# Optimization experiments

Measured on AMD Instinct MI355X. Metric: run time of the kernel, lower is better.

## Reference

```python
import jax, jax.numpy as jnp
import numpy as np

NUM_EMBEDDINGS = 8192
EMBEDDING_DIM = 256
COMMITMENT_COST = 0.25


def setup_inputs() -> dict:
    key = jax.random.key(0)
    k1, k2 = jax.random.split(key)
    inputs = jax.random.normal(k1, (16, EMBEDDING_DIM, 32, 32), dtype=jnp.float32)
    # nn.Embedding weight init: uniform(-1/num_embeddings, 1/num_embeddings)
    emb = jax.random.uniform(
        k2, (NUM_EMBEDDINGS, EMBEDDING_DIM), dtype=jnp.float32,
        minval=-1.0 / NUM_EMBEDDINGS, maxval=1.0 / NUM_EMBEDDINGS)
    return {"inputs": inputs, "emb": emb}


def reference(inputs, emb):
    # b c h w -> b h w c
    x = jnp.transpose(inputs, (0, 2, 3, 1))
    b, h, w, c = x.shape
    flat = x.reshape(-1, c)  # [N, c], N = b*h*w

    distances = (jnp.sum(flat * flat, axis=1, keepdims=True)
                 + jnp.sum(emb * emb, axis=1)
                 - 2.0 * jnp.matmul(flat, emb.T))
    encoding_indices = jnp.argmin(distances, axis=1)  # [N]
    encodings = jax.nn.one_hot(encoding_indices, NUM_EMBEDDINGS, dtype=flat.dtype)  # [N, K]

    # gather-via-matmul, as in the original
    quantized = jnp.matmul(encodings, emb).reshape(b, h, w, c)

    sg = jax.lax.stop_gradient
    e_latent_loss = jnp.mean((sg(quantized) - x) ** 2)
    q_latent_loss = jnp.mean((quantized - sg(x)) ** 2)
    loss = q_latent_loss + COMMITMENT_COST * e_latent_loss

    # straight-through estimator
    quantized_st = x + sg(quantized - x)

    avg_probs = jnp.mean(encodings, axis=0)  # [K]
    perplexity = jnp.exp(-jnp.sum(avg_probs * jnp.log(avg_probs + 1e-10)))

    # back to b c h w (intended layout of the returned quantized tensor)
    quantized_out = jnp.transpose(quantized_st, (0, 3, 1, 2))
    return loss, quantized_out, perplexity, encodings
```

## Files before the change

kernel.cpp:

```cpp
#include <hip/hip_runtime.h>
#include <math.h>

#define N_ROWS   16384
#define K_EMB    8192
#define C_DIM    256
#define QUANT_N  4194304
#define QUANT_OFF 1
#define PERP_OFF  4194305
#define ENC_OFF   4194306

#define CAND_CAP 128

#define WS_BK    0
#define WS_AN    8192
#define WS_AMIN  24576
#define WS_CCNT  57344
#define WS_CAND  73728
#define WS_IDX   4268032
#define WS_CNT   4284416
#define WS_ACC   4292608
#define WS_XH    4292616
#define WS_EH    6389768

typedef __attribute__((ext_vector_type(8))) short short8_t;
typedef __attribute__((ext_vector_type(4))) float f32x4;
typedef __attribute__((ext_vector_type(8))) unsigned short u16x8;
typedef unsigned long long ull;

__device__ __forceinline__ unsigned short f2bf(float f) {
    unsigned int u = __float_as_uint(f);
    u += 0x7FFFu + ((u >> 16) & 1u);
    return (unsigned short)(u >> 16);
}

__global__ void vq_bk_kernel(const float* __restrict__ emb, float* __restrict__ bk) {
    int row  = blockIdx.x * 4 + (threadIdx.x >> 6);
    int lane = threadIdx.x & 63;
    float4 v = reinterpret_cast<const float4*>(emb)[(size_t)row * 64 + lane];
    float s = v.x * v.x + v.y * v.y + v.z * v.z + v.w * v.w;
#pragma unroll
    for (int o = 32; o > 0; o >>= 1) s += __shfl_down(s, o, 64);
    if (lane == 0) bk[row] = s;
}

__global__ void vq_an_kernel(const float* __restrict__ xin, float* __restrict__ an) {
    int n = blockIdx.x * 256 + threadIdx.x;
    int b = n >> 10, hw = n & 1023;
    const float* xr = xin + (size_t)b * (C_DIM * 1024) + hw;
    float s = 0.f;
    for (int c = 0; c < C_DIM; ++c) { float v = xr[(size_t)c * 1024]; s = fmaf(v, v, s); }
    an[n] = s;
}

__global__ void vq_packx_kernel(const float* __restrict__ xin, unsigned short* __restrict__ xh) {
    __shared__ float tile[64][65];
    const int t = threadIdx.x;
    const int nb = blockIdx.x >> 2;
    const int cb = blockIdx.x & 3;
    const int n0 = nb * 64;
    const int b  = n0 >> 10, hw0 = n0 & 1023;
    {
        int cl = t >> 6, nl = t & 63;
#pragma unroll
        for (int i = 0; i < 16; ++i) {
            int c = cb * 64 + cl * 16 + i;
            tile[cl * 16 + i][nl] = xin[(size_t)b * (C_DIM * 1024) + (size_t)c * 1024 + hw0 + nl];
        }
    }
    __syncthreads();
    {
        int nl = t >> 2, cq = t & 3;
#pragma unroll
        for (int j = 0; j < 2; ++j) {
            u16x8 v;
#pragma unroll
            for (int jj = 0; jj < 8; ++jj) v[jj] = f2bf(tile[cq * 16 + j * 8 + jj][nl]);
            *reinterpret_cast<u16x8*>(&xh[(size_t)(n0 + nl) * 256 + cb * 64 + cq * 16 + j * 8]) = v;
        }
    }
}

__global__ void vq_packe_kernel(const float* __restrict__ emb, unsigned short* __restrict__ eh) {
    int flat = blockIdx.x * 256 + threadIdx.x;
    int k = flat >> 4, c16 = flat & 15;
    const float4* src = reinterpret_cast<const float4*>(emb) + (size_t)k * 64 + c16 * 4;
#pragma unroll
    for (int j = 0; j < 2; ++j) {
        float4 v0 = src[j * 2], v1 = src[j * 2 + 1];
        u16x8 v;
        v[0]=f2bf(v0.x); v[1]=f2bf(v0.y); v[2]=f2bf(v0.z); v[3]=f2bf(v0.w);
        v[4]=f2bf(v1.x); v[5]=f2bf(v1.y); v[6]=f2bf(v1.z); v[7]=f2bf(v1.w);
        *reinterpret_cast<u16x8*>(&eh[(size_t)k * 256 + c16 * 16 + j * 8]) = v;
    }
}

__launch_bounds__(256, 2)
__global__ void vq_mfma_kernel(const unsigned short* __restrict__ xh,
                               const unsigned short* __restrict__ eh,
                               const float* __restrict__ an,
                               const float* __restrict__ bk,
                               ull* __restrict__ amin,
                               unsigned int* __restrict__ ccnt,
                               ull* __restrict__ cand) {
    __shared__ unsigned short e_lds[256][72];
    __shared__ unsigned short x_lds[128][72];
    __shared__ ull key_lds[128][4];
    const int t  = threadIdx.x;
    const int rb = blockIdx.x >> 5;
    const int kb = blockIdx.x & 31;
    const int w  = t >> 6;
    const int l  = t & 63;
    const int lr = l & 15;
    const int lg = l >> 4;

    f32x4 acc[4][8];
#pragma unroll
    for (int kt = 0; kt < 4; ++kt)
#pragma unroll
        for (int rt = 0; rt < 8; ++rt) acc[kt][rt] = (f32x4){0.f, 0.f, 0.f, 0.f};

    const unsigned short* xbase = xh + (size_t)(rb * 128) * 256;
    const unsigned short* ebase = eh + (size_t)(kb * 256) * 256;

    for (int cc = 0; cc < 4; ++cc) {
        __syncthreads();
#pragma unroll
        for (int i = 0; i < 8; ++i) {
            int flat = t + 256 * i;
            int kr = flat >> 3, u8 = flat & 7;
            *reinterpret_cast<u16x8*>(&e_lds[kr][u8 * 8]) =
                *reinterpret_cast<const u16x8*>(&ebase[(size_t)kr * 256 + cc * 64 + u8 * 8]);
        }
#pragma unroll
        for (int i = 0; i < 4; ++i) {
            int flat = t + 256 * i;
            int xr = flat >> 3, u8 = flat & 7;
            *reinterpret_cast<u16x8*>(&x_lds[xr][u8 * 8]) =
                *reinterpret_cast<const u16x8*>(&xbase[(size_t)xr * 256 + cc * 64 + u8 * 8]);
        }
        __syncthreads();
#pragma unroll
        for (int step = 0; step < 2; ++step) {
            const int cl = step * 32 + lg * 8;
            short8_t af[4], bf[8];
#pragma unroll
            for (int kt = 0; kt < 4; ++kt)
                af[kt] = *reinterpret_cast<const short8_t*>(&e_lds[w * 64 + kt * 16 + lr][cl]);
#pragma unroll
            for (int rt = 0; rt < 8; ++rt)
                bf[rt] = *reinterpret_cast<const short8_t*>(&x_lds[rt * 16 + lr][cl]);
#pragma unroll
            for (int kt = 0; kt < 4; ++kt)
#pragma unroll
                for (int rt = 0; rt < 8; ++rt)
                    acc[kt][rt] = __builtin_amdgcn_mfma_f32_16x16x32_bf16(af[kt], bf[rt], acc[kt][rt], 0, 0, 0);
        }
    }

    float bvals[16];
#pragma unroll
    for (int kt = 0; kt < 4; ++kt)
#pragma unroll
        for (int reg = 0; reg < 4; ++reg)
            bvals[kt * 4 + reg] = bk[kb * 256 + w * 64 + kt * 16 + lg * 4 + reg];

    float ar8[8];
#pragma unroll
    for (int rt = 0; rt < 8; ++rt) {
        const int row = rb * 128 + rt * 16 + lr;
        const float a_r = an[row];
        ar8[rt] = a_r;
        float mn = 3.402823466e38f; int mk = 0;
#pragma unroll
        for (int kt = 0; kt < 4; ++kt)
#pragma unroll
            for (int reg = 0; reg < 4; ++reg) {
                float d = fmaf(-2.f, acc[kt][rt][reg], a_r + bvals[kt * 4 + reg]);
                acc[kt][rt][reg] = d;
                int k = kb * 256 + w * 64 + kt * 16 + lg * 4 + reg;
                if (d < mn) { mn = d; mk = k; }
            }
        ull key = ((ull)__float_as_uint(mn) << 32) | (unsigned)mk;
        ull o1 = __shfl_xor(key, 16, 64); if (o1 < key) key = o1;
        ull o2 = __shfl_xor(key, 32, 64); if (o2 < key) key = o2;
        if (lg == 0) {
            atomicMin(&amin[row], key);
            key_lds[rt * 16 + lr][w] = key;
        }
    }
    __syncthreads();
#pragma unroll
    for (int rt = 0; rt < 8; ++rt) {
        const int row = rb * 128 + rt * 16 + lr;
        ull bmin = key_lds[rt * 16 + lr][0];
#pragma unroll
        for (int j = 1; j < 4; ++j) { ull v = key_lds[rt * 16 + lr][j]; if (v < bmin) bmin = v; }
        ull obs = amin[row];
        if (obs < bmin) bmin = obs;
        float md  = __uint_as_float((unsigned)(bmin >> 32));
        float thr = md + fmaf(4.0e-5f, sqrtf(ar8[rt]), 1.6e-4f);
#pragma unroll
        for (int kt = 0; kt < 4; ++kt)
#pragma unroll
            for (int reg = 0; reg < 4; ++reg) {
                float d = acc[kt][rt][reg];
                if (d <= thr) {
                    int k = kb * 256 + w * 64 + kt * 16 + lg * 4 + reg;
                    unsigned pos = atomicAdd(&ccnt[row], 1u);
                    if (pos < CAND_CAP)
                        cand[(size_t)row * CAND_CAP + pos] =
                            ((ull)__float_as_uint(d) << 32) | (unsigned)k;
                }
            }
    }
}

__global__ void vq_select_kernel(const float* __restrict__ xin,
                                 const float* __restrict__ emb,
                                 const float* __restrict__ an,
                                 const float* __restrict__ bk,
                                 const ull* __restrict__ amin,
                                 const unsigned int* __restrict__ ccnt,
                                 const ull* __restrict__ cand,
                                 int* __restrict__ idx_ws,
                                 int* __restrict__ counts,
                                 float* __restrict__ enc) {
    __shared__ float xrow[4][260];
    const int w = threadIdx.x >> 6, l = threadIdx.x & 63;
    const int r = blockIdx.x * 4 + w;
    const int b = r >> 10, hw = r & 1023;
    const float* xr = xin + (size_t)b * (C_DIM * 1024) + hw;
#pragma unroll
    for (int i = 0; i < 4; ++i) xrow[w][l + 64 * i] = xr[(size_t)(l + 64 * i) * 1024];

    const unsigned cnt = ccnt[r];
    const float a_r = an[r];
    const float glob = __uint_as_float((unsigned)(amin[r] >> 32));
    const float thr  = glob + fmaf(4.0e-5f, sqrtf(a_r), 1.6e-4f);

    ull mykey = 0xFFFFFFFFFFFFFFFFull;
    if (cnt <= CAND_CAP) {
        for (unsigned i = l; i < cnt; i += 64) {
            ull e64 = cand[(size_t)r * CAND_CAP + i];
            float dt = __uint_as_float((unsigned)(e64 >> 32));
            if (dt <= thr) {
                int k = (int)(unsigned)(e64 & 0xFFFFFFFFull);
                const float* e = emb + (size_t)k * C_DIM;
                float m = 0.f;
                for (int c = 0; c < C_DIM; ++c) m = fmaf(xrow[w][c], e[c], m);
                float d = fmaf(-2.f, m, a_r + bk[k]);
                ull key = ((ull)__float_as_uint(d) << 32) | (unsigned)k;
                if (key < mykey) mykey = key;
            }
        }
    } else {
        for (int k = l; k < K_EMB; k += 64) {
            const float* e = emb + (size_t)k * C_DIM;
            float m = 0.f;
            for (int c = 0; c < C_DIM; ++c) m = fmaf(xrow[w][c], e[c], m);
            float d = fmaf(-2.f, m, a_r + bk[k]);
            ull key = ((ull)__float_as_uint(d) << 32) | (unsigned)k;
            if (key < mykey) mykey = key;
        }
    }
#pragma unroll
    for (int o = 32; o > 0; o >>= 1) {
        ull ok = __shfl_xor(mykey, o, 64);
        if (ok < mykey) mykey = ok;
    }
    if (l == 0) {
        int bi = (int)(unsigned)(mykey & 0xFFFFFFFFull);
        idx_ws[r] = bi;
        atomicAdd(&counts[bi], 1);
        enc[(size_t)r * K_EMB + bi] = 1.0f;
    }
}

__global__ void vq_quant_loss_kernel(const float* __restrict__ xin,
                                     const float* __restrict__ emb,
                                     const int* __restrict__ idx_ws,
                                     float* __restrict__ out,
                                     double* __restrict__ acc) {
    __shared__ float q_lds[64][257];
    __shared__ int   k_lds[64];
    const int tid = threadIdx.x;
    const int n0  = blockIdx.x * 64;
    const int b_img = n0 >> 10;
    const int hw0   = n0 & 1023;

    if (tid < 64) k_lds[tid] = idx_ws[n0 + tid];
    __syncthreads();
#pragma unroll
    for (int p = 0; p < 16; ++p) {
        int idx = tid + p * 256;
        int row = idx >> 6;
        int c4  = idx & 63;
        float4 q = reinterpret_cast<const float4*>(emb)[(size_t)k_lds[row] * 64 + c4];
        q_lds[row][c4 * 4 + 0] = q.x;
        q_lds[row][c4 * 4 + 1] = q.y;
        q_lds[row][c4 * 4 + 2] = q.z;
        q_lds[row][c4 * 4 + 3] = q.w;
    }
    __syncthreads();

    double local = 0.0;
    const size_t base = (size_t)b_img * (C_DIM * 1024) + hw0;
    const int hw = tid & 63;
    const int cb = tid >> 6;
    for (int pass = 0; pass < 64; ++pass) {
        int c = pass * 4 + cb;
        size_t off = base + (size_t)c * 1024 + hw;
        float x = xin[off];
        float q = q_lds[hw][c];
        float dq = q - x;
        out[QUANT_OFF + off] = x + dq;
        local += (double)dq * (double)dq;
    }
#pragma unroll
    for (int o = 32; o > 0; o >>= 1) local += __shfl_down(local, o, 64);
    __shared__ double wsum[4];
    if ((threadIdx.x & 63) == 0) wsum[threadIdx.x >> 6] = local;
    __syncthreads();
    if (threadIdx.x == 0) atomicAdd(acc, wsum[0] + wsum[1] + wsum[2] + wsum[3]);
}

__global__ void vq_finalize_kernel(const int* __restrict__ counts,
                                   const double* __restrict__ acc,
                                   float* __restrict__ out) {
    double s = 0.0;
    for (int k = threadIdx.x; k < K_EMB; k += 256) {
        int c = counts[k];
        if (c > 0) {
            double p = (double)c * (1.0 / 16384.0);
            s += p * log(p + 1e-10);
        }
    }
#pragma unroll
    for (int o = 32; o > 0; o >>= 1) s += __shfl_down(s, o, 64);
    __shared__ double wsum[4];
    if ((threadIdx.x & 63) == 0) wsum[threadIdx.x >> 6] = s;
    __syncthreads();
    if (threadIdx.x == 0) {
        double tot = wsum[0] + wsum[1] + wsum[2] + wsum[3];
        out[PERP_OFF] = (float)exp(-tot);
        float l = (float)(acc[0] * (1.0 / (double)QUANT_N));
        out[0] = l + 0.25f * l;
    }
}

extern "C" void kernel_launch(void* const* d_in, const int* in_sizes, int n_in,
                              void* d_out, int out_size, void* d_ws, size_t ws_size,
                              hipStream_t stream) {
    const float* xin = (const float*)d_in[0];
    const float* emb = (const float*)d_in[1];
    float* out = (float*)d_out;
    float* ws  = (float*)d_ws;

    float*          bk     = ws + WS_BK;
    float*          an     = ws + WS_AN;
    ull*            amin   = (ull*)(ws + WS_AMIN);
    unsigned int*   ccnt   = (unsigned int*)(ws + WS_CCNT);
    ull*            cand   = (ull*)(ws + WS_CAND);
    int*            idx_ws = (int*)(ws + WS_IDX);
    int*            counts = (int*)(ws + WS_CNT);
    double*         acc    = (double*)(ws + WS_ACC);
    unsigned short* xh     = (unsigned short*)(ws + WS_XH);
    unsigned short* eh     = (unsigned short*)(ws + WS_EH);

    hipMemsetAsync(out + ENC_OFF, 0, (size_t)N_ROWS * K_EMB * sizeof(float), stream);
    hipMemsetAsync(counts, 0, K_EMB * sizeof(int), stream);
    hipMemsetAsync(acc, 0, 16, stream);
    hipMemsetAsync(ccnt, 0, N_ROWS * sizeof(unsigned int), stream);
    hipMemsetAsync(amin, 0xFF, (size_t)N_ROWS * 8, stream);

    vq_bk_kernel<<<K_EMB / 4, 256, 0, stream>>>(emb, bk);
    vq_an_kernel<<<N_ROWS / 256, 256, 0, stream>>>(xin, an);
    vq_packx_kernel<<<(N_ROWS / 64) * 4, 256, 0, stream>>>(xin, xh);
    vq_packe_kernel<<<(K_EMB * 16) / 256, 256, 0, stream>>>(emb, eh);
    vq_mfma_kernel<<<128 * 32, 256, 0, stream>>>(xh, eh, an, bk, amin, ccnt, cand);
    vq_select_kernel<<<N_ROWS / 4, 256, 0, stream>>>(xin, emb, an, bk, amin, ccnt, cand,
                                                     idx_ws, counts, out + ENC_OFF);
    vq_quant_loss_kernel<<<N_ROWS / 64, 256, 0, stream>>>(xin, emb, idx_ws, out, acc);
    vq_finalize_kernel<<<1, 256, 0, stream>>>(counts, acc, out);
}
```

Baseline: 886.9 us.

## Fuse encodings zero-fill into MFMA kernel and replace memsets with init kernel

Removes the 512MB hipMemsetAsync of the one-hot encodings buffer. Each MFMA block now zero-fills its own 32768-float slice while it computes, so the fill overlaps compute. The small memsets are replaced by one init kernel, and the per-row atomicMin is issued once per block after the LDS reduction instead of once per wave. The select kernel loads four adjacent rows with a coalesced float4 load into a transposed LDS tile. This relies on the zero-fill in the MFMA kernel finishing before the select kernel writes the ones, which stream order guarantees.

```diff
diff --git a/kernel.cpp b/kernel.cpp
--- a/kernel.cpp
+++ b/kernel.cpp
@@ -33,6 +33,15 @@
     return (unsigned short)(u >> 16);
 }
 
+__global__ void vq_init_kernel(ull* __restrict__ amin, unsigned int* __restrict__ ccnt,
+                               int* __restrict__ counts, double* __restrict__ acc) {
+    int t = blockIdx.x * 256 + threadIdx.x;
+    amin[t] = 0xFFFFFFFFFFFFFFFFull;
+    ccnt[t] = 0u;
+    if (t < K_EMB) counts[t] = 0;
+    if (t == 0) acc[0] = 0.0;
+}
+
 __global__ void vq_bk_kernel(const float* __restrict__ emb, float* __restrict__ bk) {
     int row  = blockIdx.x * 4 + (threadIdx.x >> 6);
     int lane = threadIdx.x & 63;
@@ -101,7 +110,8 @@
                                const float* __restrict__ bk,
                                ull* __restrict__ amin,
                                unsigned int* __restrict__ ccnt,
-                               ull* __restrict__ cand) {
+                               ull* __restrict__ cand,
+                               float* __restrict__ enc) {
     __shared__ unsigned short e_lds[256][72];
     __shared__ unsigned short x_lds[128][72];
     __shared__ ull key_lds[128][4];
@@ -121,6 +131,7 @@
 
     const unsigned short* xbase = xh + (size_t)(rb * 128) * 256;
     const unsigned short* ebase = eh + (size_t)(kb * 256) * 256;
+    float2* enc_z = reinterpret_cast<float2*>(enc + (size_t)blockIdx.x * 32768);
 
     for (int cc = 0; cc < 4; ++cc) {
         __syncthreads();
@@ -138,6 +149,9 @@
             *reinterpret_cast<u16x8*>(&x_lds[xr][u8 * 8]) =
                 *reinterpret_cast<const u16x8*>(&xbase[(size_t)xr * 256 + cc * 64 + u8 * 8]);
         }
+#pragma unroll
+        for (int z = 0; z < 16; ++z)
+            enc_z[(cc * 16 + z) * 256 + t] = (float2){0.f, 0.f};
         __syncthreads();
 #pragma unroll
         for (int step = 0; step < 2; ++step) {
@@ -183,10 +197,7 @@
         ull key = ((ull)__float_as_uint(mn) << 32) | (unsigned)mk;
         ull o1 = __shfl_xor(key, 16, 64); if (o1 < key) key = o1;
         ull o2 = __shfl_xor(key, 32, 64); if (o2 < key) key = o2;
-        if (lg == 0) {
-            atomicMin(&amin[row], key);
-            key_lds[rt * 16 + lr][w] = key;
-        }
+        if (lg == 0) key_lds[rt * 16 + lr][w] = key;
     }
     __syncthreads();
 #pragma unroll
@@ -195,6 +206,7 @@
         ull bmin = key_lds[rt * 16 + lr][0];
 #pragma unroll
         for (int j = 1; j < 4; ++j) { ull v = key_lds[rt * 16 + lr][j]; if (v < bmin) bmin = v; }
+        if (w == 0 && lg == 0) atomicMin(&amin[row], bmin);
         ull obs = amin[row];
         if (obs < bmin) bmin = obs;
         float md  = __uint_as_float((unsigned)(bmin >> 32));
@@ -225,14 +237,19 @@
                                  int* __restrict__ idx_ws,
                                  int* __restrict__ counts,
                                  float* __restrict__ enc) {
-    __shared__ float xrow[4][260];
-    const int w = threadIdx.x >> 6, l = threadIdx.x & 63;
-    const int r = blockIdx.x * 4 + w;
-    const int b = r >> 10, hw = r & 1023;
-    const float* xr = xin + (size_t)b * (C_DIM * 1024) + hw;
-#pragma unroll
-    for (int i = 0; i < 4; ++i) xrow[w][l + 64 * i] = xr[(size_t)(l + 64 * i) * 1024];
-
+    __shared__ float xrow4[256][4];
+    const int t = threadIdx.x;
+    const int w = t >> 6, l = t & 63;
+    const int n0 = blockIdx.x * 4;
+    const int b  = n0 >> 10, hw0 = n0 & 1023;
+    {
+        float4 v = *reinterpret_cast<const float4*>(
+            xin + (size_t)b * (C_DIM * 1024) + (size_t)t * 1024 + hw0);
+        xrow4[t][0] = v.x; xrow4[t][1] = v.y; xrow4[t][2] = v.z; xrow4[t][3] = v.w;
+    }
+    __syncthreads();
+
+    const int r = n0 + w;
     const unsigned cnt = ccnt[r];
     const float a_r = an[r];
     const float glob = __uint_as_float((unsigned)(amin[r] >> 32));
@@ -247,7 +264,7 @@
                 int k = (int)(unsigned)(e64 & 0xFFFFFFFFull);
                 const float* e = emb + (size_t)k * C_DIM;
                 float m = 0.f;
-                for (int c = 0; c < C_DIM; ++c) m = fmaf(xrow[w][c], e[c], m);
+                for (int c = 0; c < C_DIM; ++c) m = fmaf(xrow4[c][w], e[c], m);
                 float d = fmaf(-2.f, m, a_r + bk[k]);
                 ull key = ((ull)__float_as_uint(d) << 32) | (unsigned)k;
                 if (key < mykey) mykey = key;
@@ -257,7 +274,7 @@
         for (int k = l; k < K_EMB; k += 64) {
             const float* e = emb + (size_t)k * C_DIM;
             float m = 0.f;
-            for (int c = 0; c < C_DIM; ++c) m = fmaf(xrow[w][c], e[c], m);
+            for (int c = 0; c < C_DIM; ++c) m = fmaf(xrow4[c][w], e[c], m);
             float d = fmaf(-2.f, m, a_r + bk[k]);
             ull key = ((ull)__float_as_uint(d) << 32) | (unsigned)k;
             if (key < mykey) mykey = key;
@@ -367,17 +384,12 @@
     unsigned short* xh     = (unsigned short*)(ws + WS_XH);
     unsigned short* eh     = (unsigned short*)(ws + WS_EH);
 
-    hipMemsetAsync(out + ENC_OFF, 0, (size_t)N_ROWS * K_EMB * sizeof(float), stream);
-    hipMemsetAsync(counts, 0, K_EMB * sizeof(int), stream);
-    hipMemsetAsync(acc, 0, 16, stream);
-    hipMemsetAsync(ccnt, 0, N_ROWS * sizeof(unsigned int), stream);
-    hipMemsetAsync(amin, 0xFF, (size_t)N_ROWS * 8, stream);
-
+    vq_init_kernel<<<64, 256, 0, stream>>>(amin, ccnt, counts, acc);
     vq_bk_kernel<<<K_EMB / 4, 256, 0, stream>>>(emb, bk);
     vq_an_kernel<<<N_ROWS / 256, 256, 0, stream>>>(xin, an);
+    vq_packe_kernel<<<(K_EMB * 16) / 256, 256, 0, stream>>>(emb, eh);
     vq_packx_kernel<<<(N_ROWS / 64) * 4, 256, 0, stream>>>(xin, xh);
-    vq_packe_kernel<<<(K_EMB * 16) / 256, 256, 0, stream>>>(emb, eh);
-    vq_mfma_kernel<<<128 * 32, 256, 0, stream>>>(xh, eh, an, bk, amin, ccnt, cand);
+    vq_mfma_kernel<<<128 * 32, 256, 0, stream>>>(xh, eh, an, bk, amin, ccnt, cand, out + ENC_OFF);
     vq_select_kernel<<<N_ROWS / 4, 256, 0, stream>>>(xin, emb, an, bk, amin, ccnt, cand,
                                                      idx_ws, counts, out + ENC_OFF);
     vq_quant_loss_kernel<<<N_ROWS / 64, 256, 0, stream>>>(xin, emb, idx_ws, out, acc);
```

Measured after the change: 937.0 us. 5.6% more time.
